# Performance work log

Measured on AMD Instinct MI355X. Metric: run time of the kernel, lower is better.

The kernel has to match this reference:

```python
import jax, jax.numpy as jnp
import numpy as np

NEG_INF = -1e6  # d2l masked_softmax fill value


def setup_inputs() -> dict:
    key = jax.random.key(0)
    kq, kk, kv, kl = jax.random.split(key, 4)
    n, s, d = 32, 2048, 64
    queries = jax.random.normal(kq, (n, s, d), dtype=jnp.float32)
    keys = jax.random.normal(kk, (n, s, d), dtype=jnp.float32)
    values = jax.random.normal(kv, (n, s, d), dtype=jnp.float32)
    valid_lens = jax.random.randint(kl, (n,), 1, s + 1, dtype=jnp.int32)
    return {"queries": queries, "keys": keys, "values": values, "valid_lens": valid_lens}


def reference(queries, keys, values, valid_lens):
    d = queries.shape[-1]
    # scores: [n, q, k]
    scores = jnp.einsum("nqd,nkd->nqk", queries, keys) / jnp.sqrt(jnp.float32(d))
    kv_len = scores.shape[-1]
    # masked_softmax: positions >= valid_len get NEG_INF before softmax
    mask = jnp.arange(kv_len, dtype=jnp.int32)[None, None, :] < valid_lens[:, None, None]
    scores = jnp.where(mask, scores, NEG_INF)
    attn = jax.nn.softmax(scores, axis=-1)
    # dropout rate 0.0 (inference) -> identity
    return jnp.einsum("nqk,nkd->nqd", attn, values)
```

## Files before the change

### kernel.cpp

```cpp
#include <hip/hip_runtime.h>
#include <hip/hip_bf16.h>


typedef short bf16x8 __attribute__((ext_vector_type(8)));
typedef float f32x4  __attribute__((ext_vector_type(4)));
typedef unsigned int u32;
typedef u32 u32x2 __attribute__((ext_vector_type(2)));

#define SEQ 2048
#define DH 64
#define BK 64
#define LDSP 72
#define SCLQ 0.18033688011112042f

static __device__ __forceinline__ short f2bf(float f) {
    unsigned u = __float_as_uint(f);
    return (short)((u + 0x7FFFu + ((u >> 16) & 1u)) >> 16);
}
static __device__ __forceinline__ u32 pk2bf(float lo, float hi) {
    __hip_bfloat162 h = __float22bfloat162_rn(float2{lo, hi});
    return *(u32*)&h;
}

__global__ __launch_bounds__(256, 4)
void attn_fwd(const float* __restrict__ Q,
              const float* __restrict__ K,
              const float* __restrict__ V,
              const int* __restrict__ VL,
              float* __restrict__ O)
{
    __shared__ short Klds[BK][LDSP];
    __shared__ short Vt[DH][LDSP];
    __shared__ short Plds[4][16][LDSP];
    __shared__ int   Rsort[32];

    const int tid  = threadIdx.x;
    const int wave = tid >> 6;
    const int lane = tid & 63;
    const int g    = lane >> 4;
    const int l15  = lane & 15;

    if (tid < 32) {
        const int nv = (VL[tid] + BK - 1) >> 6;
        int rank = 0;
        for (int jj = 0; jj < 32; ++jj) {
            const int nj = (VL[jj] + BK - 1) >> 6;
            rank += (nj > nv) || (nj == nv && jj < tid);
        }
        Rsort[rank] = tid;
    }
    __syncthreads();

    const int jb = blockIdx.x & 255;
    const int sl = blockIdx.x >> 8;
    const int c  = jb >> 5;
    const int qt = jb & 31;
    const int rk = (sl == 0) ? c : (sl == 1) ? (15 - c)
                 : (sl == 2) ? (16 + c) : (31 - c);
    const int b  = Rsort[rk];

    const int vl  = VL[b];
    const int nkt = (vl + BK - 1) >> 6;

    const size_t bo = (size_t)b * SEQ * DH;
    const float* Qb = Q + bo;
    const float* Kb = K + bo;
    const float* Vb = V + bo;

    const int qrow = qt * 64 + wave * 16 + l15;
    bf16x8 aq0, aq1;
    {
        const float* qp = Qb + (size_t)qrow * DH + g * 8;
        f32x4 q0 = *(const f32x4*)(qp);
        f32x4 q1 = *(const f32x4*)(qp + 4);
        f32x4 q2 = *(const f32x4*)(qp + 32);
        f32x4 q3 = *(const f32x4*)(qp + 36);
        #pragma unroll
        for (int j = 0; j < 4; ++j) {
            aq0[j]     = f2bf(q0[j] * SCLQ);
            aq0[j + 4] = f2bf(q1[j] * SCLQ);
            aq1[j]     = f2bf(q2[j] * SCLQ);
            aq1[j + 4] = f2bf(q3[j] * SCLQ);
        }
    }

    bf16x8 ones;
    #pragma unroll
    for (int j = 0; j < 8; ++j) ones[j] = (short)0x3F80;

    f32x4 oacc[4];
    #pragma unroll
    for (int i = 0; i < 4; ++i) oacc[i] = f32x4{0.f, 0.f, 0.f, 0.f};
    f32x4 lacc = f32x4{0.f, 0.f, 0.f, 0.f};

    f32x4 kpre[4], vpre[4];
    #pragma unroll
    for (int h = 0; h < 4; ++h) {
        const int cc = tid + h * 256;
        kpre[h] = *(const f32x4*)(Kb + (size_t)(cc >> 4) * DH + (cc & 15) * 4);
    }
    #pragma unroll
    for (int h = 0; h < 2; ++h) {
        const float* src = Vb + (size_t)lane * DH + wave * 8 + h * 32;
        vpre[2 * h]     = *(const f32x4*)(src);
        vpre[2 * h + 1] = *(const f32x4*)(src + 4);
    }

    for (int kt = 0; kt < nkt; ++kt) {
        const int k0 = kt * BK;

        #pragma unroll
        for (int h = 0; h < 4; ++h) {
            const int cc = tid + h * 256;
            u32x2 o;
            o[0] = pk2bf(kpre[h][0], kpre[h][1]);
            o[1] = pk2bf(kpre[h][2], kpre[h][3]);
            *(u32x2*)(&Klds[cc >> 4][(cc & 15) * 4]) = o;
        }
        #pragma unroll
        for (int h = 0; h < 2; ++h) {
            const int d0 = wave * 8 + h * 32;
            const u32 p0 = pk2bf(vpre[2 * h][0],     vpre[2 * h][1]);
            const u32 p1 = pk2bf(vpre[2 * h][2],     vpre[2 * h][3]);
            const u32 p2 = pk2bf(vpre[2 * h + 1][0], vpre[2 * h + 1][1]);
            const u32 p3 = pk2bf(vpre[2 * h + 1][2], vpre[2 * h + 1][3]);
            Vt[d0 + 0][lane] = (short)(p0);  Vt[d0 + 1][lane] = (short)(p0 >> 16);
            Vt[d0 + 2][lane] = (short)(p1);  Vt[d0 + 3][lane] = (short)(p1 >> 16);
            Vt[d0 + 4][lane] = (short)(p2);  Vt[d0 + 5][lane] = (short)(p2 >> 16);
            Vt[d0 + 6][lane] = (short)(p3);  Vt[d0 + 7][lane] = (short)(p3 >> 16);
        }
        __syncthreads();

        if (kt + 1 < nkt) {
            const int kn = k0 + BK;
            #pragma unroll
            for (int h = 0; h < 4; ++h) {
                const int cc = tid + h * 256;
                kpre[h] = *(const f32x4*)(Kb + (size_t)(kn + (cc >> 4)) * DH + (cc & 15) * 4);
            }
            #pragma unroll
            for (int h = 0; h < 2; ++h) {
                const float* src = Vb + (size_t)(kn + lane) * DH + wave * 8 + h * 32;
                vpre[2 * h]     = *(const f32x4*)(src);
                vpre[2 * h + 1] = *(const f32x4*)(src + 4);
            }
        }

        f32x4 s[4];
        #pragma unroll
        for (int nb = 0; nb < 4; ++nb) {
            bf16x8 bk0 = *(const bf16x8*)(&Klds[nb * 16 + l15][g * 8]);
            bf16x8 bk1 = *(const bf16x8*)(&Klds[nb * 16 + l15][32 + g * 8]);
            f32x4 acc = f32x4{0.f, 0.f, 0.f, 0.f};
            acc = __builtin_amdgcn_mfma_f32_16x16x32_bf16(aq0, bk0, acc, 0, 0, 0);
            acc = __builtin_amdgcn_mfma_f32_16x16x32_bf16(aq1, bk1, acc, 0, 0, 0);
            s[nb] = acc;
        }

        if (k0 + BK <= vl) {
            #pragma unroll
            for (int nb = 0; nb < 4; ++nb)
                #pragma unroll
                for (int r = 0; r < 4; ++r)
                    s[nb][r] = __builtin_amdgcn_exp2f(s[nb][r]);
        } else {
            #pragma unroll
            for (int nb = 0; nb < 4; ++nb) {
                const bool ok = (k0 + nb * 16 + l15) < vl;
                #pragma unroll
                for (int r = 0; r < 4; ++r)
                    s[nb][r] = ok ? __builtin_amdgcn_exp2f(s[nb][r]) : 0.f;
            }
        }

        #pragma unroll
        for (int nb = 0; nb < 4; ++nb) {
            const u32 p01 = pk2bf(s[nb][0], s[nb][1]);
            const u32 p23 = pk2bf(s[nb][2], s[nb][3]);
            Plds[wave][g * 4 + 0][nb * 16 + l15] = (short)(p01);
            Plds[wave][g * 4 + 1][nb * 16 + l15] = (short)(p01 >> 16);
            Plds[wave][g * 4 + 2][nb * 16 + l15] = (short)(p23);
            Plds[wave][g * 4 + 3][nb * 16 + l15] = (short)(p23 >> 16);
        }
        asm volatile("" ::: "memory");

        #pragma unroll
        for (int cc = 0; cc < 2; ++cc) {
            bf16x8 ap = *(const bf16x8*)(&Plds[wave][l15][cc * 32 + g * 8]);
            lacc = __builtin_amdgcn_mfma_f32_16x16x32_bf16(ap, ones, lacc, 0, 0, 0);
            #pragma unroll
            for (int db = 0; db < 4; ++db) {
                bf16x8 bv = *(const bf16x8*)(&Vt[db * 16 + l15][cc * 32 + g * 8]);
                oacc[db] = __builtin_amdgcn_mfma_f32_16x16x32_bf16(ap, bv, oacc[db], 0, 0, 0);
            }
        }
        __syncthreads();
    }

    #pragma unroll
    for (int r = 0; r < 4; ++r) {
        const float inv = 1.0f / lacc[r];
        const int row = qt * 64 + wave * 16 + g * 4 + r;
        #pragma unroll
        for (int db = 0; db < 4; ++db)
            O[bo + (size_t)row * DH + db * 16 + l15] = oacc[db][r] * inv;
    }
}

extern "C" void kernel_launch(void* const* d_in, const int* in_sizes, int n_in,
                              void* d_out, int out_size, void* d_ws, size_t ws_size,
                              hipStream_t stream) {
    const float* Q  = (const float*)d_in[0];
    const float* K  = (const float*)d_in[1];
    const float* V  = (const float*)d_in[2];
    const int*   VL = (const int*)d_in[3];
    float* O = (float*)d_out;

    dim3 grid(1024);
    dim3 block(256);
    attn_fwd<<<grid, block, 0, stream>>>(Q, K, V, VL, O);
}
```

Baseline: 132.8 us.

## Precompute bf16 K and transposed V in a prepass kernel

Adds a prepass kernel that converts K to bf16 and writes V transposed as bf16 into workspace. The attention kernel then loads half as many bytes per tile and copies them straight into LDS with no per-block conversion or scalar transposed stores. The QK MFMA operand order is swapped so that P is written as packed 64-bit LDS stores. The cost is an extra launch plus a full read and write of K and V in the prepass. The old fp32 path is kept as a fallback when the workspace is too small.

After: 127.7 us. 1.04x faster.

```diff
diff --git a/kernel.cpp b/kernel.cpp
--- a/kernel.cpp
+++ b/kernel.cpp
@@ -6,6 +6,7 @@
 typedef float f32x4  __attribute__((ext_vector_type(4)));
 typedef unsigned int u32;
 typedef u32 u32x2 __attribute__((ext_vector_type(2)));
+typedef u32 u32x4 __attribute__((ext_vector_type(4)));
 
 #define SEQ 2048
 #define DH 64
@@ -23,15 +24,66 @@
 }
 
 __global__ __launch_bounds__(256, 4)
+void prepass(const float* __restrict__ K, const float* __restrict__ V,
+             short* __restrict__ Kbf, short* __restrict__ Vt)
+{
+    __shared__ short T[DH][LDSP];
+
+    const int tid  = threadIdx.x;
+    const int wave = tid >> 6;
+    const int lane = tid & 63;
+    const int b  = blockIdx.x & 31;
+    const int kt = blockIdx.x >> 5;
+    const int k0 = kt * BK;
+    const size_t bo = (size_t)b * SEQ * DH;
+
+    const float* Ks = K + bo + (size_t)k0 * DH;
+    u32* Kd = (u32*)(Kbf + bo + (size_t)k0 * DH);
+    #pragma unroll
+    for (int h = 0; h < 2; ++h) {
+        const int c2 = tid + h * 256;
+        f32x4 a = *(const f32x4*)(Ks + c2 * 8);
+        f32x4 c = *(const f32x4*)(Ks + c2 * 8 + 4);
+        u32x4 o;
+        o[0] = pk2bf(a[0], a[1]); o[1] = pk2bf(a[2], a[3]);
+        o[2] = pk2bf(c[0], c[1]); o[3] = pk2bf(c[2], c[3]);
+        *(u32x4*)(Kd + c2 * 4) = o;
+    }
+
+    #pragma unroll
+    for (int h = 0; h < 2; ++h) {
+        const int d0 = wave * 8 + h * 32;
+        const float* src = V + bo + (size_t)(k0 + lane) * DH + d0;
+        f32x4 va = *(const f32x4*)(src);
+        f32x4 vb = *(const f32x4*)(src + 4);
+        #pragma unroll
+        for (int j = 0; j < 4; ++j) {
+            T[d0 + j][lane]     = f2bf(va[j]);
+            T[d0 + 4 + j][lane] = f2bf(vb[j]);
+        }
+    }
+    __syncthreads();
+
+    short* Vd = Vt + (size_t)b * DH * SEQ;
+    #pragma unroll
+    for (int h = 0; h < 2; ++h) {
+        const int c2 = tid + h * 256;
+        const int d  = c2 >> 3;
+        const int kc = (c2 & 7) * 8;
+        *(bf16x8*)(Vd + (size_t)d * SEQ + k0 + kc) = *(const bf16x8*)(&T[d][kc]);
+    }
+}
+
+template <bool PRE>
+__global__ __launch_bounds__(256, 4)
 void attn_fwd(const float* __restrict__ Q,
-              const float* __restrict__ K,
-              const float* __restrict__ V,
-              const int* __restrict__ VL,
-              float* __restrict__ O)
+              const float* __restrict__ Kf, const float* __restrict__ Vf,
+              const short* __restrict__ Kbf, const short* __restrict__ Vtg,
+              const int* __restrict__ VL, float* __restrict__ O)
 {
     __shared__ short Klds[BK][LDSP];
     __shared__ short Vt[DH][LDSP];
-    __shared__ short Plds[4][16][LDSP];
+    __shared__ short Pw[4][16][LDSP];
     __shared__ int   Rsort[32];
 
     const int tid  = threadIdx.x;
@@ -53,24 +105,25 @@
 
     const int jb = blockIdx.x & 255;
     const int sl = blockIdx.x >> 8;
-    const int c  = jb >> 5;
+    const int c8 = jb >> 5;
     const int qt = jb & 31;
-    const int rk = (sl == 0) ? c : (sl == 1) ? (15 - c)
-                 : (sl == 2) ? (16 + c) : (31 - c);
+    const int rk = (sl == 0) ? c8 : (sl == 1) ? (15 - c8)
+                 : (sl == 2) ? (16 + c8) : (31 - c8);
     const int b  = Rsort[rk];
 
     const int vl  = VL[b];
     const int nkt = (vl + BK - 1) >> 6;
 
     const size_t bo = (size_t)b * SEQ * DH;
-    const float* Qb = Q + bo;
-    const float* Kb = K + bo;
-    const float* Vb = V + bo;
+    const short* Kb = Kbf + bo;
+    const short* Vb = Vtg + (size_t)b * DH * SEQ;
+    const float* Kbf32 = Kf + bo;
+    const float* Vbf32 = Vf + bo;
 
     const int qrow = qt * 64 + wave * 16 + l15;
     bf16x8 aq0, aq1;
     {
-        const float* qp = Qb + (size_t)qrow * DH + g * 8;
+        const float* qp = Q + bo + (size_t)qrow * DH + g * 8;
         f32x4 q0 = *(const f32x4*)(qp);
         f32x4 q1 = *(const f32x4*)(qp + 4);
         f32x4 q2 = *(const f32x4*)(qp + 32);
@@ -93,67 +146,92 @@
     for (int i = 0; i < 4; ++i) oacc[i] = f32x4{0.f, 0.f, 0.f, 0.f};
     f32x4 lacc = f32x4{0.f, 0.f, 0.f, 0.f};
 
-    f32x4 kpre[4], vpre[4];
-    #pragma unroll
-    for (int h = 0; h < 4; ++h) {
-        const int cc = tid + h * 256;
-        kpre[h] = *(const f32x4*)(Kb + (size_t)(cc >> 4) * DH + (cc & 15) * 4);
-    }
-    #pragma unroll
-    for (int h = 0; h < 2; ++h) {
-        const float* src = Vb + (size_t)lane * DH + wave * 8 + h * 32;
-        vpre[2 * h]     = *(const f32x4*)(src);
-        vpre[2 * h + 1] = *(const f32x4*)(src + 4);
+    bf16x8 kpre[2], vpre[2];
+    f32x4 kpre32[4], vpre32[4];
+    if (PRE) {
+        #pragma unroll
+        for (int h = 0; h < 2; ++h) {
+            const int c2 = tid + h * 256;
+            kpre[h] = *(const bf16x8*)(Kb + c2 * 8);
+            vpre[h] = *(const bf16x8*)(Vb + (size_t)(c2 >> 3) * SEQ + ((c2 & 7) * 8));
+        }
+    } else {
+        #pragma unroll
+        for (int h = 0; h < 4; ++h) {
+            const int cc = tid + h * 256;
+            kpre32[h] = *(const f32x4*)(Kbf32 + (size_t)(cc >> 4) * DH + (cc & 15) * 4);
+        }
+        #pragma unroll
+        for (int h = 0; h < 2; ++h) {
+            const float* src = Vbf32 + (size_t)lane * DH + wave * 8 + h * 32;
+            vpre32[2 * h]     = *(const f32x4*)(src);
+            vpre32[2 * h + 1] = *(const f32x4*)(src + 4);
+        }
     }
 
     for (int kt = 0; kt < nkt; ++kt) {
         const int k0 = kt * BK;
 
-        #pragma unroll
-        for (int h = 0; h < 4; ++h) {
-            const int cc = tid + h * 256;
-            u32x2 o;
-            o[0] = pk2bf(kpre[h][0], kpre[h][1]);
-            o[1] = pk2bf(kpre[h][2], kpre[h][3]);
-            *(u32x2*)(&Klds[cc >> 4][(cc & 15) * 4]) = o;
-        }
-        #pragma unroll
-        for (int h = 0; h < 2; ++h) {
-            const int d0 = wave * 8 + h * 32;
-            const u32 p0 = pk2bf(vpre[2 * h][0],     vpre[2 * h][1]);
-            const u32 p1 = pk2bf(vpre[2 * h][2],     vpre[2 * h][3]);
-            const u32 p2 = pk2bf(vpre[2 * h + 1][0], vpre[2 * h + 1][1]);
-            const u32 p3 = pk2bf(vpre[2 * h + 1][2], vpre[2 * h + 1][3]);
-            Vt[d0 + 0][lane] = (short)(p0);  Vt[d0 + 1][lane] = (short)(p0 >> 16);
-            Vt[d0 + 2][lane] = (short)(p1);  Vt[d0 + 3][lane] = (short)(p1 >> 16);
-            Vt[d0 + 4][lane] = (short)(p2);  Vt[d0 + 5][lane] = (short)(p2 >> 16);
-            Vt[d0 + 6][lane] = (short)(p3);  Vt[d0 + 7][lane] = (short)(p3 >> 16);
+        if (PRE) {
+            #pragma unroll
+            for (int h = 0; h < 2; ++h) {
+                const int c2 = tid + h * 256;
+                *(bf16x8*)(&Klds[c2 >> 3][(c2 & 7) * 8]) = kpre[h];
+                *(bf16x8*)(&Vt[c2 >> 3][(c2 & 7) * 8])   = vpre[h];
+            }
+        } else {
+            #pragma unroll
+            for (int h = 0; h < 4; ++h) {
+                const int cc = tid + h * 256;
+                u32x2 o;
+                o[0] = pk2bf(kpre32[h][0], kpre32[h][1]);
+                o[1] = pk2bf(kpre32[h][2], kpre32[h][3]);
+                *(u32x2*)(&Klds[cc >> 4][(cc & 15) * 4]) = o;
+            }
+            #pragma unroll
+            for (int h = 0; h < 2; ++h) {
+                const int d0 = wave * 8 + h * 32;
+                #pragma unroll
+                for (int j = 0; j < 4; ++j) {
+                    Vt[d0 + j][lane]     = f2bf(vpre32[2 * h][j]);
+                    Vt[d0 + 4 + j][lane] = f2bf(vpre32[2 * h + 1][j]);
+                }
+            }
         }
         __syncthreads();
 
         if (kt + 1 < nkt) {
             const int kn = k0 + BK;
-            #pragma unroll
-            for (int h = 0; h < 4; ++h) {
-                const int cc = tid + h * 256;
-                kpre[h] = *(const f32x4*)(Kb + (size_t)(kn + (cc >> 4)) * DH + (cc & 15) * 4);
-            }
-            #pragma unroll
-            for (int h = 0; h < 2; ++h) {
-                const float* src = Vb + (size_t)(kn + lane) * DH + wave * 8 + h * 32;
-                vpre[2 * h]     = *(const f32x4*)(src);
-                vpre[2 * h + 1] = *(const f32x4*)(src + 4);
+            if (PRE) {
+                #pragma unroll
+                for (int h = 0; h < 2; ++h) {
+                    const int c2 = tid + h * 256;
+                    kpre[h] = *(const bf16x8*)(Kb + (size_t)kn * DH + c2 * 8);
+                    vpre[h] = *(const bf16x8*)(Vb + (size_t)(c2 >> 3) * SEQ + kn + ((c2 & 7) * 8));
+                }
+            } else {
+                #pragma unroll
+                for (int h = 0; h < 4; ++h) {
+                    const int cc = tid + h * 256;
+                    kpre32[h] = *(const f32x4*)(Kbf32 + (size_t)(kn + (cc >> 4)) * DH + (cc & 15) * 4);
+                }
+                #pragma unroll
+                for (int h = 0; h < 2; ++h) {
+                    const float* src = Vbf32 + (size_t)(kn + lane) * DH + wave * 8 + h * 32;
+                    vpre32[2 * h]     = *(const f32x4*)(src);
+                    vpre32[2 * h + 1] = *(const f32x4*)(src + 4);
+                }
             }
         }
 
         f32x4 s[4];
         #pragma unroll
         for (int nb = 0; nb < 4; ++nb) {
-            bf16x8 bk0 = *(const bf16x8*)(&Klds[nb * 16 + l15][g * 8]);
-            bf16x8 bk1 = *(const bf16x8*)(&Klds[nb * 16 + l15][32 + g * 8]);
+            bf16x8 ak0 = *(const bf16x8*)(&Klds[nb * 16 + l15][g * 8]);
+            bf16x8 ak1 = *(const bf16x8*)(&Klds[nb * 16 + l15][32 + g * 8]);
             f32x4 acc = f32x4{0.f, 0.f, 0.f, 0.f};
-            acc = __builtin_amdgcn_mfma_f32_16x16x32_bf16(aq0, bk0, acc, 0, 0, 0);
-            acc = __builtin_amdgcn_mfma_f32_16x16x32_bf16(aq1, bk1, acc, 0, 0, 0);
+            acc = __builtin_amdgcn_mfma_f32_16x16x32_bf16(ak0, aq0, acc, 0, 0, 0);
+            acc = __builtin_amdgcn_mfma_f32_16x16x32_bf16(ak1, aq1, acc, 0, 0, 0);
             s[nb] = acc;
         }
 
@@ -165,28 +243,26 @@
                     s[nb][r] = __builtin_amdgcn_exp2f(s[nb][r]);
         } else {
             #pragma unroll
-            for (int nb = 0; nb < 4; ++nb) {
-                const bool ok = (k0 + nb * 16 + l15) < vl;
-                #pragma unroll
-                for (int r = 0; r < 4; ++r)
+            for (int nb = 0; nb < 4; ++nb)
+                #pragma unroll
+                for (int r = 0; r < 4; ++r) {
+                    const bool ok = (k0 + nb * 16 + g * 4 + r) < vl;
                     s[nb][r] = ok ? __builtin_amdgcn_exp2f(s[nb][r]) : 0.f;
-            }
+                }
         }
 
         #pragma unroll
         for (int nb = 0; nb < 4; ++nb) {
-            const u32 p01 = pk2bf(s[nb][0], s[nb][1]);
-            const u32 p23 = pk2bf(s[nb][2], s[nb][3]);
-            Plds[wave][g * 4 + 0][nb * 16 + l15] = (short)(p01);
-            Plds[wave][g * 4 + 1][nb * 16 + l15] = (short)(p01 >> 16);
-            Plds[wave][g * 4 + 2][nb * 16 + l15] = (short)(p23);
-            Plds[wave][g * 4 + 3][nb * 16 + l15] = (short)(p23 >> 16);
+            u32x2 pkv;
+            pkv[0] = pk2bf(s[nb][0], s[nb][1]);
+            pkv[1] = pk2bf(s[nb][2], s[nb][3]);
+            *(u32x2*)(&Pw[wave][l15][nb * 16 + g * 4]) = pkv;
         }
         asm volatile("" ::: "memory");
 
         #pragma unroll
         for (int cc = 0; cc < 2; ++cc) {
-            bf16x8 ap = *(const bf16x8*)(&Plds[wave][l15][cc * 32 + g * 8]);
+            bf16x8 ap = *(const bf16x8*)(&Pw[wave][l15][cc * 32 + g * 8]);
             lacc = __builtin_amdgcn_mfma_f32_16x16x32_bf16(ap, ones, lacc, 0, 0, 0);
             #pragma unroll
             for (int db = 0; db < 4; ++db) {
@@ -216,7 +292,14 @@
     const int*   VL = (const int*)d_in[3];
     float* O = (float*)d_out;
 
-    dim3 grid(1024);
-    dim3 block(256);
-    attn_fwd<<<grid, block, 0, stream>>>(Q, K, V, VL, O);
-}
+    const size_t nel = (size_t)32 * SEQ * DH;
+    const size_t need = 2 * nel * sizeof(short);
+    if (ws_size >= need) {
+        short* Kbf = (short*)d_ws;
+        short* Vt  = Kbf + nel;
+        prepass<<<dim3(1024), dim3(256), 0, stream>>>(K, V, Kbf, Vt);
+        attn_fwd<true><<<dim3(1024), dim3(256), 0, stream>>>(Q, K, V, Kbf, Vt, VL, O);
+    } else {
+        attn_fwd<false><<<dim3(1024), dim3(256), 0, stream>>>(Q, K, V, nullptr, nullptr, VL, O);
+    }
+}
```
